# Optimization experiments

Measured on AMD Instinct MI355X. Metric: run time of the kernel, lower is better.

## Reference

```python
import jax, jax.numpy as jnp
import numpy as np

B, H, W, C = 8, 64, 64, 256
NH, WS, SS = 8, 8, 4
HD = C // NH          # head dim 32
N = WS * WS           # 64 tokens per window
NW = (H // WS) * (W // WS)  # 64 windows
MLP = 4 * C


def _rel_index():
    ch = np.arange(WS)
    coords = np.stack(np.meshgrid(ch, ch, indexing='ij')).reshape(2, -1)  # [2, N]
    rel = (coords[:, :, None] - coords[:, None, :]).transpose(1, 2, 0)   # [N, N, 2]
    rel[:, :, 0] += WS - 1
    rel[:, :, 1] += WS - 1
    rel[:, :, 0] *= 2 * WS - 1
    return jnp.asarray(rel.sum(-1))  # [N, N] indices into table

REL_IDX = _rel_index()


def _attn_mask():
    # standard Swin shifted-window mask: [nW, N, N] with 0 / -100
    img = np.zeros((H, W))
    slices = (slice(0, -WS), slice(-WS, -SS), slice(-SS, None))
    cnt = 0
    for hs in slices:
        for ws_ in slices:
            img[hs, ws_] = cnt
            cnt += 1
    m = img.reshape(H // WS, WS, W // WS, WS).transpose(0, 2, 1, 3).reshape(-1, N)
    diff = m[:, None, :] - m[:, :, None]
    return jnp.asarray(np.where(diff != 0, -100.0, 0.0).astype(np.float32))

MASK = _attn_mask()


def setup_inputs() -> dict:
    key = jax.random.key(0)
    ks = jax.random.split(key, 8)
    s = 0.02
    return {
        'hidden_states': jax.random.normal(ks[0], (B, H * W, C), jnp.float32),
        'ln1_g': jnp.ones((C,), jnp.float32),
        'ln1_b': jnp.zeros((C,), jnp.float32),
        'wq': jax.random.normal(ks[1], (C, C), jnp.float32) * s,
        'bq': jnp.zeros((C,), jnp.float32),
        'wk': jax.random.normal(ks[2], (C, C), jnp.float32) * s,
        'bk': jnp.zeros((C,), jnp.float32),
        'wv': jax.random.normal(ks[3], (C, C), jnp.float32) * s,
        'bv': jnp.zeros((C,), jnp.float32),
        'rel_table': jax.random.normal(ks[4], ((2 * WS - 1) ** 2, NH), jnp.float32) * s,
        'wo': jax.random.normal(ks[5], (C, C), jnp.float32) * s,
        'bo': jnp.zeros((C,), jnp.float32),
        'ln2_g': jnp.ones((C,), jnp.float32),
        'ln2_b': jnp.zeros((C,), jnp.float32),
        'w1': jax.random.normal(ks[6], (MLP, C), jnp.float32) * s,
        'b1': jnp.zeros((MLP,), jnp.float32),
        'w2': jax.random.normal(ks[7], (C, MLP), jnp.float32) * s,
        'b2': jnp.zeros((C,), jnp.float32),
    }


def _ln(x, g, b):
    mu = x.mean(-1, keepdims=True)
    var = x.var(-1, keepdims=True)
    return (x - mu) * jax.lax.rsqrt(var + 1e-5) * g + b


def reference(hidden_states, ln1_g, ln1_b, wq, bq, wk, bk, wv, bv, rel_table,
              wo, bo, ln2_g, ln2_b, w1, b1, w2, b2):
    shortcut = hidden_states
    x = _ln(hidden_states, ln1_g, ln1_b).reshape(B, H, W, C)
    # cyclic shift
    x = jnp.roll(x, (-SS, -SS), axis=(1, 2))
    # window partition -> [B*nW, N, C]
    xw = x.reshape(B, H // WS, WS, W // WS, WS, C).transpose(0, 1, 3, 2, 4, 5).reshape(-1, N, C)
    q = (xw @ wq.T + bq).reshape(-1, N, NH, HD).transpose(0, 2, 1, 3)
    k = (xw @ wk.T + bk).reshape(-1, N, NH, HD).transpose(0, 2, 1, 3)
    v = (xw @ wv.T + bv).reshape(-1, N, NH, HD).transpose(0, 2, 1, 3)
    scores = jnp.einsum('bhnd,bhmd->bhnm', q, k) / np.float32(np.sqrt(HD))
    bias = rel_table[REL_IDX]                 # [N, N, NH] gathered bias
    scores = scores + bias.transpose(2, 0, 1)[None]
    scores = scores.reshape(B, NW, NH, N, N) + MASK[None, :, None]
    probs = jax.nn.softmax(scores, axis=-1).reshape(-1, NH, N, N)
    ctx = jnp.einsum('bhnm,bhmd->bnhd', probs, v).reshape(-1, N, C)
    attn_out = ctx @ wo.T + bo                # SelfOutput dense
    # window reverse + reverse shift
    x = attn_out.reshape(B, H // WS, W // WS, WS, WS, C).transpose(0, 1, 3, 2, 4, 5).reshape(B, H, W, C)
    x = jnp.roll(x, (SS, SS), axis=(1, 2)).reshape(B, H * W, C)
    hidden = shortcut + x
    y = _ln(hidden, ln2_g, ln2_b)
    y = jax.nn.gelu(y @ w1.T + b1, approximate=False) @ w2.T + b2
    return hidden + y
```

## Files before the change

### kernel.cpp

```cpp
#include <hip/hip_runtime.h>
#include <hip/hip_bf16.h>
#include <math.h>

__device__ __forceinline__ unsigned short f2bf(float f) {
    union { float f; unsigned u; } c; c.f = f;
    unsigned r = c.u + 0x7fffu + ((c.u >> 16) & 1u);
    return (unsigned short)(r >> 16);
}
__device__ __forceinline__ float bfu(unsigned short u) {
    union { unsigned x; float f; } c; c.x = ((unsigned)u) << 16; return c.f;
}
__device__ __forceinline__ float gelu_t(float x) {
    float z = x * (1.59576912f + 0.07135481f * x * x);
    return x / (1.0f + __expf(-z));
}

typedef __bf16 bf16x8_t __attribute__((ext_vector_type(8)));
typedef float  f32x4_t  __attribute__((ext_vector_type(4)));
typedef unsigned short u16x8 __attribute__((ext_vector_type(8)));

#define AS1 __attribute__((address_space(1)))
#define AS3 __attribute__((address_space(3)))
__device__ __forceinline__ void g2lds16(const void* g, void* l) {
    __builtin_amdgcn_global_load_lds((const AS1 unsigned int*)g, (AS3 unsigned int*)l, 16, 0, 0);
}

__global__ void cvt_all(const float* __restrict__ wq, const float* __restrict__ wk,
                        const float* __restrict__ wv, const float* __restrict__ wo,
                        const float* __restrict__ w1, const float* __restrict__ w2,
                        const float* __restrict__ bq, const float* __restrict__ bk,
                        const float* __restrict__ bv, float* __restrict__ bqkv,
                        unsigned short* __restrict__ qkvp, unsigned short* __restrict__ wop,
                        unsigned short* __restrict__ w1p, unsigned short* __restrict__ w2p) {
    int fid = blockIdx.x * 256 + threadIdx.x;
    if (fid >= 98304) {
        int i = fid - 98304;
        if (i < 768) bqkv[i] = (i < 256) ? bq[i] : (i < 512 ? bk[i - 256] : bv[i - 512]);
        return;
    }
    const float* src; unsigned short* dst; int n, kf, KC;
    if (fid < 24576) {
        n = fid >> 5; kf = fid & 31; KC = 8;
        const float* w = (n < 256) ? wq : (n < 512 ? wk : wv);
        src = w + (size_t)(n & 255) * 256 + kf * 8; dst = qkvp;
    } else if (fid < 32768) {
        int fi = fid - 24576; n = fi >> 5; kf = fi & 31; KC = 8;
        src = wo + (size_t)n * 256 + kf * 8; dst = wop;
    } else if (fid < 65536) {
        int fi = fid - 32768; n = fi >> 5; kf = fi & 31; KC = 8;
        src = w1 + (size_t)n * 256 + kf * 8; dst = w1p;
    } else {
        int fi = fid - 65536; n = fi >> 7; kf = fi & 127; KC = 32;
        src = w2 + (size_t)n * 1024 + kf * 8; dst = w2p;
    }
    size_t oidx = (size_t)(((n >> 7) * KC + (kf >> 2)) * 4096)
                + ((n >> 4) & 7) * 512 + (kf & 3) * 128 + (n & 15) * 8;
    float4 a = *(const float4*)(src);
    float4 b = *(const float4*)(src + 4);
    u16x8 o = { f2bf(a.x), f2bf(a.y), f2bf(a.z), f2bf(a.w),
                f2bf(b.x), f2bf(b.y), f2bf(b.z), f2bf(b.w) };
    *(u16x8*)(dst + oidx) = o;
}

template<int GATHER, int BF16IN>
__global__ void ln_kernel(const void* __restrict__ xv, const float* __restrict__ g,
                          const float* __restrict__ b, unsigned short* __restrict__ out) {
    int row  = blockIdx.x * 4 + (threadIdx.x >> 6);
    int lane = threadIdx.x & 63;
    int src;
    if (GATHER) {
        int bb = row >> 12;
        int rem = row & 4095;
        int winid = rem >> 6, tok = rem & 63;
        int wi = winid >> 3, wj = winid & 7;
        int ii = tok >> 3,  jj = tok & 7;
        int hh = (wi * 8 + ii + 4) & 63;
        int ww = (wj * 8 + jj + 4) & 63;
        src = (bb << 12) + hh * 64 + ww;
    } else {
        src = row;
    }
    float4 v;
    if (BF16IN) {
        ushort4 u = *(const ushort4*)((const unsigned short*)xv + (size_t)src * 256 + lane * 4);
        v.x = bfu(u.x); v.y = bfu(u.y); v.z = bfu(u.z); v.w = bfu(u.w);
    } else {
        v = *(const float4*)((const float*)xv + (size_t)src * 256 + lane * 4);
    }
    float s  = v.x + v.y + v.z + v.w;
    float s2 = v.x*v.x + v.y*v.y + v.z*v.z + v.w*v.w;
    #pragma unroll
    for (int off = 32; off > 0; off >>= 1) {
        s  += __shfl_xor(s,  off, 64);
        s2 += __shfl_xor(s2, off, 64);
    }
    float mean = s * (1.0f / 256.0f);
    float var  = s2 * (1.0f / 256.0f) - mean * mean;
    float rstd = rsqrtf(var + 1e-5f);
    int c0 = lane * 4;
    float4 gg  = *(const float4*)(g + c0);
    float4 bb4 = *(const float4*)(b + c0);
    ushort4 o;
    o.x = f2bf((v.x - mean) * rstd * gg.x + bb4.x);
    o.y = f2bf((v.y - mean) * rstd * gg.y + bb4.y);
    o.z = f2bf((v.z - mean) * rstd * gg.z + bb4.z);
    o.w = f2bf((v.w - mean) * rstd * gg.w + bb4.w);
    *(ushort4*)(out + (size_t)row * 256 + c0) = o;
}

template<int MODE, int K>
__global__ __launch_bounds__(256, 4) void gemm_tile(
        const unsigned short* __restrict__ A,
        const unsigned short* __restrict__ Bp,
        const float* __restrict__ bias,
        int M, int N,
        unsigned short* __restrict__ obf,
        float* __restrict__ of32,
        const void* __restrict__ addp) {
    __shared__ __align__(16) char smem_raw[64 * 132 * 4];
    unsigned short* sm = (unsigned short*)smem_raw;
    float* cst = (float*)smem_raw;
    const int t = threadIdx.x;
    const int lane = t & 63, wave = t >> 6;
    const int m0 = blockIdx.x * 128, n0 = blockIdx.y * 128;
    const int wm = (wave >> 1) * 64, wn = (wave & 1) * 64;
    const int lr = lane & 15, kg = lane >> 4;

    f32x4_t acc[4][4];
    #pragma unroll
    for (int i = 0; i < 4; ++i)
        #pragma unroll
        for (int j = 0; j < 4; ++j) { acc[i][j][0]=0.f; acc[i][j][1]=0.f; acc[i][j][2]=0.f; acc[i][j][3]=0.f; }

    const unsigned short* ga  = A  + (size_t)(m0 + (t >> 2)) * K + (t & 3) * 8;
    const unsigned short* gbp = Bp + (size_t)blockIdx.y * (K / 32) * 4096 + t * 8;
    unsigned short* lA = sm + t * 8;
    unsigned short* lB = sm + 4096 + t * 8;

    const int NT = K / 32;
    g2lds16(ga,                  lA);
    g2lds16(ga + (size_t)64 * K, lA + 2048);
    g2lds16(gbp,                 lB);
    g2lds16(gbp + 2048,          lB + 2048);
    __syncthreads();

    #pragma unroll
    for (int k = 0; k < NT; ++k) {
        const int cur = k & 1;
        if (k + 1 < NT) {
            const int nx = cur ^ 1;
            g2lds16(ga + (k + 1) * 32,                  lA + nx * 8192);
            g2lds16(ga + (size_t)64 * K + (k + 1) * 32, lA + nx * 8192 + 2048);
            g2lds16(gbp + (size_t)(k + 1) * 4096,        lB + nx * 8192);
            g2lds16(gbp + (size_t)(k + 1) * 4096 + 2048, lB + nx * 8192 + 2048);
        }
        const unsigned short* Ab = sm + cur * 8192;
        const unsigned short* Bb = Ab + 4096;
        bf16x8_t af[4], bfr[4];
        #pragma unroll
        for (int i = 0; i < 4; ++i)
            af[i] = *(const bf16x8_t*)&Ab[(wm + i * 16 + lr) * 32 + kg * 8];
        #pragma unroll
        for (int j = 0; j < 4; ++j)
            bfr[j] = *(const bf16x8_t*)&Bb[(((wave & 1) * 4 + j) * 64 + lane) * 8];
        #pragma unroll
        for (int i = 0; i < 4; ++i)
            #pragma unroll
            for (int j = 0; j < 4; ++j)
                acc[i][j] = __builtin_amdgcn_mfma_f32_16x16x32_bf16(af[i], bfr[j], acc[i][j], 0, 0, 0);
        __syncthreads();
    }

    #pragma unroll
    for (int pass = 0; pass < 2; ++pass) {
        if (pass) __syncthreads();
        if ((wave >> 1) == pass) {
            float* cw = cst + (kg * 4) * 132 + wn + lr;
            #pragma unroll
            for (int i = 0; i < 4; ++i)
                #pragma unroll
                for (int j = 0; j < 4; ++j)
                    #pragma unroll
                    for (int e = 0; e < 4; ++e)
                        cw[(i * 16 + e) * 132 + j * 16] = acc[i][j][e];
        }
        __syncthreads();
        const int rr = t >> 4;
        const int ch = t & 15;
        if (MODE == 0 || MODE == 1) {
            #pragma unroll
            for (int c = 0; c < 4; ++c) {
                int r = rr + c * 16;
                int grow = m0 + pass * 64 + r;
                const float* cr = cst + r * 132 + ch * 8;
                const float* bp = bias + n0 + ch * 8;
                float4 a   = *(const float4*)(cr);
                float4 b4  = *(const float4*)(cr + 4);
                float4 ba  = *(const float4*)(bp);
                float4 bb4 = *(const float4*)(bp + 4);
                float x0 = a.x + ba.x,  x1 = a.y + ba.y,  x2 = a.z + ba.z,  x3 = a.w + ba.w;
                float x4 = b4.x + bb4.x, x5 = b4.y + bb4.y, x6 = b4.z + bb4.z, x7 = b4.w + bb4.w;
                if (MODE == 1) {
                    x0 = gelu_t(x0); x1 = gelu_t(x1); x2 = gelu_t(x2); x3 = gelu_t(x3);
                    x4 = gelu_t(x4); x5 = gelu_t(x5); x6 = gelu_t(x6); x7 = gelu_t(x7);
                }
                u16x8 o = { f2bf(x0), f2bf(x1), f2bf(x2), f2bf(x3),
                            f2bf(x4), f2bf(x5), f2bf(x6), f2bf(x7) };
                *(u16x8*)(obf + (size_t)grow * N + n0 + ch * 8) = o;
            }
        } else if (MODE == 2) {
            #pragma unroll
            for (int c = 0; c < 4; ++c) {
                int r = rr + c * 16;
                int grow = m0 + pass * 64 + r;
                int bb_ = grow >> 12, rem = grow & 4095;
                int winid = rem >> 6, tok = rem & 63;
                int wi = winid >> 3, wj = winid & 7;
                int ii = tok >> 3,  jj = tok & 7;
                int hh = (wi * 8 + ii + 4) & 63;
                int ww = (wj * 8 + jj + 4) & 63;
                size_t drow = (size_t)(bb_ << 12) + hh * 64 + ww;
                const float* cr = cst + r * 132 + ch * 8;
                const float* bp = bias + n0 + ch * 8;
                const float* res = (const float*)addp + drow * N + n0 + ch * 8;
                float4 a   = *(const float4*)(cr);
                float4 b4  = *(const float4*)(cr + 4);
                float4 ba  = *(const float4*)(bp);
                float4 bb4 = *(const float4*)(bp + 4);
                float4 ra  = *(const float4*)(res);
                float4 rb  = *(const float4*)(res + 4);
                u16x8 o = { f2bf(a.x + ba.x + ra.x),  f2bf(a.y + ba.y + ra.y),
                            f2bf(a.z + ba.z + ra.z),  f2bf(a.w + ba.w + ra.w),
                            f2bf(b4.x + bb4.x + rb.x), f2bf(b4.y + bb4.y + rb.y),
                            f2bf(b4.z + bb4.z + rb.z), f2bf(b4.w + bb4.w + rb.w) };
                *(u16x8*)(obf + drow * N + n0 + ch * 8) = o;
            }
        } else {
            #pragma unroll
            for (int c = 0; c < 8; ++c) {
                int r = rr + (c & 3) * 16;
                int grow = m0 + pass * 64 + r;
                int chunk = ch + (c >> 2) * 16;
                const float* cr = cst + r * 132 + chunk * 4;
                const float* bp = bias + n0 + chunk * 4;
                const unsigned short* res = (const unsigned short*)addp + (size_t)grow * N + n0 + chunk * 4;
                float4 a  = *(const float4*)(cr);
                float4 ba = *(const float4*)(bp);
                ushort4 rv = *(const ushort4*)(res);
                float4 o1 = { bfu(rv.x) + a.x + ba.x,  bfu(rv.y) + a.y + ba.y,
                              bfu(rv.z) + a.z + ba.z,  bfu(rv.w) + a.w + ba.w };
                *(float4*)(of32 + (size_t)grow * N + n0 + chunk * 4) = o1;
            }
        }
    }
}

#define PR 72
#define VR 72
__global__ void __launch_bounds__(256) attn_mfma(
        const unsigned short* __restrict__ qkv,
        const float* __restrict__ relt,
        unsigned short* __restrict__ ctx) {
    __shared__ float rs[1800];
    __shared__ unsigned short Pl[4][64 * PR];
    __shared__ unsigned short Vt[4][32 * VR];

    int t = threadIdx.x;
    int lane = t & 63, wave = t >> 6;
    for (int i = t; i < 1800; i += 256) rs[i] = relt[i];
    __syncthreads();

    int wh = blockIdx.x * 4 + wave;
    int wg = wh >> 3, h = wh & 7;
    int win = wg & 63;
    int ln = lane & 15, quad = lane >> 4;

    unsigned short* P = &Pl[wave][0];
    unsigned short* V = &Vt[wave][0];
    const unsigned short* base = qkv + (size_t)wg * 64 * 768 + h * 32;

    union BF8 { bf16x8_t v; unsigned short s[8]; };
    {
        const bf16x8_t* vp = (const bf16x8_t*)(base + (size_t)lane * 768 + 512);
        BF8 vv[4];
        #pragma unroll
        for (int c = 0; c < 4; ++c) vv[c].v = vp[c];
        #pragma unroll
        for (int c = 0; c < 4; ++c)
            #pragma unroll
            for (int e = 0; e < 8; ++e)
                V[(c * 8 + e) * VR + lane] = vv[c].s[e];
    }

    bf16x8_t qa[4], kb[4];
    #pragma unroll
    for (int i = 0; i < 4; ++i)
        qa[i] = *(const bf16x8_t*)(base + (size_t)(i * 16 + ln) * 768 + quad * 8);
    #pragma unroll
    for (int j = 0; j < 4; ++j)
        kb[j] = *(const bf16x8_t*)(base + (size_t)(j * 16 + ln) * 768 + 256 + quad * 8);

    f32x4_t acc[4][4];
    #pragma unroll
    for (int i = 0; i < 4; ++i)
        #pragma unroll
        for (int j = 0; j < 4; ++j) { acc[i][j][0]=0.f; acc[i][j][1]=0.f; acc[i][j][2]=0.f; acc[i][j][3]=0.f; }
    #pragma unroll
    for (int i = 0; i < 4; ++i)
        #pragma unroll
        for (int j = 0; j < 4; ++j)
            acc[i][j] = __builtin_amdgcn_mfma_f32_16x16x32_bf16(qa[i], kb[j], acc[i][j], 0, 0, 0);

    const float scale = 0.17677669529663687f;
    int wi = win >> 3, wj = win & 7;
    int mjv = ln & 7;
    int regm[4], mi[4];
    #pragma unroll
    for (int j = 0; j < 4; ++j) {
        mi[j] = j * 2 + (ln >> 3);
        int hm = wi * 8 + mi[j], wm = wj * 8 + mjv;
        regm[j] = (hm < 56 ? 0 : (hm < 60 ? 1 : 2)) * 3 + (wm < 56 ? 0 : (wm < 60 ? 1 : 2));
    }
    float inv[4][4];
    #pragma unroll
    for (int i = 0; i < 4; ++i) {
        #pragma unroll
        for (int e = 0; e < 4; ++e) {
            int q = i * 16 + quad * 4 + e;
            int ti = q >> 3, tj = q & 7;
            int hn = wi * 8 + ti, wn = wj * 8 + tj;
            int regn = (hn < 56 ? 0 : (hn < 60 ? 1 : 2)) * 3 + (wn < 56 ? 0 : (wn < 60 ? 1 : 2));
            float sum = 0.f;
            #pragma unroll
            for (int j = 0; j < 4; ++j) {
                float bv = rs[((ti - mi[j] + 7) * 15 + (tj - mjv + 7)) * 8 + h];
                float sv = acc[i][j][e] * scale + bv + (regm[j] != regn ? -100.f : 0.f);
                float p = __expf(sv);
                sum += p;
                P[q * PR + j * 16 + ln] = f2bf(p);
            }
            #pragma unroll
            for (int off = 1; off < 16; off <<= 1) sum += __shfl_xor(sum, off, 64);
            inv[i][e] = 1.0f / sum;
        }
    }
    __syncthreads();

    bf16x8_t vb[2][2];
    #pragma unroll
    for (int jd = 0; jd < 2; ++jd)
        #pragma unroll
        for (int kc = 0; kc < 2; ++kc)
            vb[jd][kc] = *(const bf16x8_t*)&V[(jd * 16 + ln) * VR + kc * 32 + quad * 8];
    f32x4_t occ[4][2];
    #pragma unroll
    for (int i = 0; i < 4; ++i)
        #pragma unroll
        for (int jd = 0; jd < 2; ++jd) { occ[i][jd][0]=0.f; occ[i][jd][1]=0.f; occ[i][jd][2]=0.f; occ[i][jd][3]=0.f; }
    #pragma unroll
    for (int i = 0; i < 4; ++i) {
        #pragma unroll
        for (int kc = 0; kc < 2; ++kc) {
            bf16x8_t pf = *(const bf16x8_t*)&P[(i * 16 + ln) * PR + kc * 32 + quad * 8];
            occ[i][0] = __builtin_amdgcn_mfma_f32_16x16x32_bf16(pf, vb[0][kc], occ[i][0], 0, 0, 0);
            occ[i][1] = __builtin_amdgcn_mfma_f32_16x16x32_bf16(pf, vb[1][kc], occ[i][1], 0, 0, 0);
        }
    }

    unsigned short* cbase = ctx + (size_t)wg * 64 * 256 + h * 32;
    #pragma unroll
    for (int i = 0; i < 4; ++i)
        #pragma unroll
        for (int e = 0; e < 4; ++e) {
            int q = i * 16 + quad * 4 + e;
            #pragma unroll
            for (int jd = 0; jd < 2; ++jd)
                cbase[(size_t)q * 256 + jd * 16 + ln] = f2bf(occ[i][jd][e] * inv[i][e]);
        }
}

extern "C" void kernel_launch(void* const* d_in, const int* in_sizes, int n_in,
                              void* d_out, int out_size, void* d_ws, size_t ws_size,
                              hipStream_t stream) {
    const float* hs   = (const float*)d_in[0];
    const float* ln1g = (const float*)d_in[1];
    const float* ln1b = (const float*)d_in[2];
    const float* wq   = (const float*)d_in[3];
    const float* bq   = (const float*)d_in[4];
    const float* wk   = (const float*)d_in[5];
    const float* bk   = (const float*)d_in[6];
    const float* wv   = (const float*)d_in[7];
    const float* bv   = (const float*)d_in[8];
    const float* relt = (const float*)d_in[9];
    const float* wo   = (const float*)d_in[10];
    const float* bo   = (const float*)d_in[11];
    const float* ln2g = (const float*)d_in[12];
    const float* ln2b = (const float*)d_in[13];
    const float* w1   = (const float*)d_in[14];
    const float* b1   = (const float*)d_in[15];
    const float* w2   = (const float*)d_in[16];
    const float* b2   = (const float*)d_in[17];
    float* out = (float*)d_out;

    const size_t NTOK = 32768;
    size_t off = 0;
    auto carve = [&](size_t bytes) { void* p = (char*)d_ws + off; off += (bytes + 255) & ~(size_t)255; return p; };
    unsigned short* wqkv_p = (unsigned short*)carve(768ull * 256 * 2);
    unsigned short* wo_p   = (unsigned short*)carve(65536ull * 2);
    unsigned short* w1p    = (unsigned short*)carve(262144ull * 2);
    unsigned short* w2p    = (unsigned short*)carve(262144ull * 2);
    float*          bqkv   = (float*)carve(768ull * 4);
    unsigned short* hiddenb= (unsigned short*)carve(NTOK * 256 * 2);
    unsigned short* xw     = (unsigned short*)carve(NTOK * 256 * 2);
    unsigned short* qkvb   = (unsigned short*)carve(NTOK * 768 * 2);
    unsigned short* cx     = (unsigned short*)carve(NTOK * 256 * 2);
    unsigned short* h1 = qkvb;
    unsigned short* yb = xw;

    cvt_all<<<385, 256, 0, stream>>>(wq, wk, wv, wo, w1, w2, bq, bk, bv, bqkv,
                                     wqkv_p, wo_p, w1p, w2p);

    ln_kernel<1, 0><<<8192, 256, 0, stream>>>(hs, ln1g, ln1b, xw);

    gemm_tile<0, 256><<<dim3(256, 6), 256, 0, stream>>>(xw, wqkv_p, bqkv, 32768, 768, qkvb, nullptr, nullptr);

    attn_mfma<<<1024, 256, 0, stream>>>(qkvb, relt, cx);

    gemm_tile<2, 256><<<dim3(256, 2), 256, 0, stream>>>(cx, wo_p, bo, 32768, 256, hiddenb, nullptr, hs);

    ln_kernel<0, 1><<<8192, 256, 0, stream>>>(hiddenb, ln2g, ln2b, yb);

    gemm_tile<1, 256><<<dim3(256, 8), 256, 0, stream>>>(yb, w1p, b1, 32768, 1024, h1, nullptr, nullptr);

    gemm_tile<3, 1024><<<dim3(256, 2), 256, 0, stream>>>(h1, w2p, b2, 32768, 256, nullptr, out, hiddenb);
}
```

Baseline: 246.1 us.

## Fold LN2 into the MLP up-projection GEMM and write head-major QKV layout

After: 259.9 us. 5.6% more time.

```diff
diff --git a/kernel.cpp b/kernel.cpp
--- a/kernel.cpp
+++ b/kernel.cpp
@@ -28,6 +28,7 @@
 __global__ void cvt_all(const float* __restrict__ wq, const float* __restrict__ wk,
                         const float* __restrict__ wv, const float* __restrict__ wo,
                         const float* __restrict__ w1, const float* __restrict__ w2,
+                        const float* __restrict__ ln2g,
                         const float* __restrict__ bq, const float* __restrict__ bk,
                         const float* __restrict__ bv, float* __restrict__ bqkv,
                         unsigned short* __restrict__ qkvp, unsigned short* __restrict__ wop,
@@ -38,7 +39,7 @@
         if (i < 768) bqkv[i] = (i < 256) ? bq[i] : (i < 512 ? bk[i - 256] : bv[i - 512]);
         return;
     }
-    const float* src; unsigned short* dst; int n, kf, KC;
+    const float* src; unsigned short* dst; int n, kf, KC, isw1 = 0;
     if (fid < 24576) {
         n = fid >> 5; kf = fid & 31; KC = 8;
         const float* w = (n < 256) ? wq : (n < 512 ? wk : wv);
@@ -48,7 +49,7 @@
         src = wo + (size_t)n * 256 + kf * 8; dst = wop;
     } else if (fid < 65536) {
         int fi = fid - 32768; n = fi >> 5; kf = fi & 31; KC = 8;
-        src = w1 + (size_t)n * 256 + kf * 8; dst = w1p;
+        src = w1 + (size_t)n * 256 + kf * 8; dst = w1p; isw1 = 1;
     } else {
         int fi = fid - 65536; n = fi >> 7; kf = fi & 127; KC = 32;
         src = w2 + (size_t)n * 1024 + kf * 8; dst = w2p;
@@ -57,9 +58,34 @@
                 + ((n >> 4) & 7) * 512 + (kf & 3) * 128 + (n & 15) * 8;
     float4 a = *(const float4*)(src);
     float4 b = *(const float4*)(src + 4);
+    if (isw1) {
+        int k0 = kf * 8;
+        float4 g0 = *(const float4*)(ln2g + k0);
+        float4 g1 = *(const float4*)(ln2g + k0 + 4);
+        a.x *= g0.x; a.y *= g0.y; a.z *= g0.z; a.w *= g0.w;
+        b.x *= g1.x; b.y *= g1.y; b.z *= g1.z; b.w *= g1.w;
+    }
     u16x8 o = { f2bf(a.x), f2bf(a.y), f2bf(a.z), f2bf(a.w),
                 f2bf(b.x), f2bf(b.y), f2bf(b.z), f2bf(b.w) };
     *(u16x8*)(dst + oidx) = o;
+}
+
+__global__ void prep_mlp(const float* __restrict__ w1, const float* __restrict__ ln2g,
+                         const float* __restrict__ ln2b, const float* __restrict__ b1,
+                         float* __restrict__ s1, float* __restrict__ b1p) {
+    int n = blockIdx.x * 256 + threadIdx.x;
+    const float* wr = w1 + (size_t)n * 256;
+    float ss = 0.f, sb = 0.f;
+    #pragma unroll 4
+    for (int k = 0; k < 256; k += 4) {
+        float4 w = *(const float4*)(wr + k);
+        float4 g = *(const float4*)(ln2g + k);
+        float4 b = *(const float4*)(ln2b + k);
+        ss += w.x * g.x + w.y * g.y + w.z * g.z + w.w * g.w;
+        sb += w.x * b.x + w.y * b.y + w.z * b.z + w.w * b.w;
+    }
+    s1[n] = ss;
+    b1p[n] = b1[n] + sb;
 }
 
 template<int GATHER, int BF16IN>
@@ -117,14 +143,35 @@
         unsigned short* __restrict__ obf,
         float* __restrict__ of32,
         const void* __restrict__ addp) {
-    __shared__ __align__(16) char smem_raw[64 * 132 * 4];
+    __shared__ __align__(16) char smem_raw[34816];
     unsigned short* sm = (unsigned short*)smem_raw;
     float* cst = (float*)smem_raw;
+    float* stats = (float*)(smem_raw + 33792);
     const int t = threadIdx.x;
     const int lane = t & 63, wave = t >> 6;
     const int m0 = blockIdx.x * 128, n0 = blockIdx.y * 128;
     const int wm = (wave >> 1) * 64, wn = (wave & 1) * 64;
     const int lr = lane & 15, kg = lane >> 4;
+
+    if (MODE == 5) {
+        const unsigned short* xp = A + (size_t)(m0 + (t >> 1)) * 256 + (t & 1) * 128;
+        float s = 0.f, s2 = 0.f;
+        #pragma unroll
+        for (int f = 0; f < 16; ++f) {
+            u16x8 xf = *(const u16x8*)(xp + f * 8);
+            #pragma unroll
+            for (int e = 0; e < 8; ++e) { float v = bfu(xf[e]); s += v; s2 += v * v; }
+        }
+        s  += __shfl_xor(s, 1, 64);
+        s2 += __shfl_xor(s2, 1, 64);
+        if ((t & 1) == 0) {
+            float mean = s * (1.0f / 256.0f);
+            float var  = s2 * (1.0f / 256.0f) - mean * mean;
+            float rst  = rsqrtf(var + 1e-5f);
+            stats[t >> 1] = rst;
+            stats[128 + (t >> 1)] = mean * rst;
+        }
+    }
 
     f32x4_t acc[4][4];
     #pragma unroll
@@ -187,7 +234,7 @@
         __syncthreads();
         const int rr = t >> 4;
         const int ch = t & 15;
-        if (MODE == 0 || MODE == 1) {
+        if (MODE == 0) {
             #pragma unroll
             for (int c = 0; c < 4; ++c) {
                 int r = rr + c * 16;
@@ -198,12 +245,53 @@
                 float4 b4  = *(const float4*)(cr + 4);
                 float4 ba  = *(const float4*)(bp);
                 float4 bb4 = *(const float4*)(bp + 4);
-                float x0 = a.x + ba.x,  x1 = a.y + ba.y,  x2 = a.z + ba.z,  x3 = a.w + ba.w;
-                float x4 = b4.x + bb4.x, x5 = b4.y + bb4.y, x6 = b4.z + bb4.z, x7 = b4.w + bb4.w;
-                if (MODE == 1) {
-                    x0 = gelu_t(x0); x1 = gelu_t(x1); x2 = gelu_t(x2); x3 = gelu_t(x3);
-                    x4 = gelu_t(x4); x5 = gelu_t(x5); x6 = gelu_t(x6); x7 = gelu_t(x7);
-                }
+                u16x8 o = { f2bf(a.x + ba.x),  f2bf(a.y + ba.y),  f2bf(a.z + ba.z),  f2bf(a.w + ba.w),
+                            f2bf(b4.x + bb4.x), f2bf(b4.y + bb4.y), f2bf(b4.z + bb4.z), f2bf(b4.w + bb4.w) };
+                *(u16x8*)(obf + (size_t)grow * N + n0 + ch * 8) = o;
+            }
+        } else if (MODE == 4) {
+            #pragma unroll
+            for (int c = 0; c < 4; ++c) {
+                int r = rr + c * 16;
+                int grow = m0 + pass * 64 + r;
+                int wgq = grow >> 6, tok = grow & 63;
+                int cc = n0 + ch * 8;
+                int sel = cc >> 8, hh = (cc >> 5) & 7, d = cc & 31;
+                size_t dst = ((size_t)(wgq * 3 + sel) * 8 + hh) * 2048 + tok * 32 + d;
+                const float* cr = cst + r * 132 + ch * 8;
+                const float* bp = bias + cc;
+                float4 a   = *(const float4*)(cr);
+                float4 b4  = *(const float4*)(cr + 4);
+                float4 ba  = *(const float4*)(bp);
+                float4 bb4 = *(const float4*)(bp + 4);
+                u16x8 o = { f2bf(a.x + ba.x),  f2bf(a.y + ba.y),  f2bf(a.z + ba.z),  f2bf(a.w + ba.w),
+                            f2bf(b4.x + bb4.x), f2bf(b4.y + bb4.y), f2bf(b4.z + bb4.z), f2bf(b4.w + bb4.w) };
+                *(u16x8*)(obf + dst) = o;
+            }
+        } else if (MODE == 5) {
+            #pragma unroll
+            for (int c = 0; c < 4; ++c) {
+                int r = rr + c * 16;
+                int grow = m0 + pass * 64 + r;
+                float rst = stats[pass * 64 + r];
+                float mrs = stats[128 + pass * 64 + r];
+                const float* cr = cst + r * 132 + ch * 8;
+                const float* bp = bias + n0 + ch * 8;
+                const float* sp = (const float*)addp + n0 + ch * 8;
+                float4 a   = *(const float4*)(cr);
+                float4 b4  = *(const float4*)(cr + 4);
+                float4 ba  = *(const float4*)(bp);
+                float4 bb4 = *(const float4*)(bp + 4);
+                float4 sa  = *(const float4*)(sp);
+                float4 sb  = *(const float4*)(sp + 4);
+                float x0 = gelu_t(rst * a.x - mrs * sa.x + ba.x);
+                float x1 = gelu_t(rst * a.y - mrs * sa.y + ba.y);
+                float x2 = gelu_t(rst * a.z - mrs * sa.z + ba.z);
+                float x3 = gelu_t(rst * a.w - mrs * sa.w + ba.w);
+                float x4 = gelu_t(rst * b4.x - mrs * sb.x + bb4.x);
+                float x5 = gelu_t(rst * b4.y - mrs * sb.y + bb4.y);
+                float x6 = gelu_t(rst * b4.z - mrs * sb.z + bb4.z);
+                float x7 = gelu_t(rst * b4.w - mrs * sb.w + bb4.w);
                 u16x8 o = { f2bf(x0), f2bf(x1), f2bf(x2), f2bf(x3),
                             f2bf(x4), f2bf(x5), f2bf(x6), f2bf(x7) };
                 *(u16x8*)(obf + (size_t)grow * N + n0 + ch * 8) = o;
@@ -277,11 +365,13 @@
 
     unsigned short* P = &Pl[wave][0];
     unsigned short* V = &Vt[wave][0];
-    const unsigned short* base = qkv + (size_t)wg * 64 * 768 + h * 32;
+    const unsigned short* bq_ = qkv + ((size_t)(wg * 3 + 0) * 8 + h) * 2048;
+    const unsigned short* bk_ = qkv + ((size_t)(wg * 3 + 1) * 8 + h) * 2048;
+    const unsigned short* bv_ = qkv + ((size_t)(wg * 3 + 2) * 8 + h) * 2048;
 
     union BF8 { bf16x8_t v; unsigned short s[8]; };
     {
-        const bf16x8_t* vp = (const bf16x8_t*)(base + (size_t)lane * 768 + 512);
+        const bf16x8_t* vp = (const bf16x8_t*)(bv_ + (size_t)lane * 32);
         BF8 vv[4];
         #pragma unroll
         for (int c = 0; c < 4; ++c) vv[c].v = vp[c];
@@ -295,10 +385,10 @@
     bf16x8_t qa[4], kb[4];
     #pragma unroll
     for (int i = 0; i < 4; ++i)
-        qa[i] = *(const bf16x8_t*)(base + (size_t)(i * 16 + ln) * 768 + quad * 8);
+        qa[i] = *(const bf16x8_t*)(bq_ + (size_t)(i * 16 + ln) * 32 + quad * 8);
     #pragma unroll
     for (int j = 0; j < 4; ++j)
-        kb[j] = *(const bf16x8_t*)(base + (size_t)(j * 16 + ln) * 768 + 256 + quad * 8);
+        kb[j] = *(const bf16x8_t*)(bk_ + (size_t)(j * 16 + ln) * 32 + quad * 8);
 
     f32x4_t acc[4][4];
     #pragma unroll
@@ -410,27 +500,27 @@
     unsigned short* w1p    = (unsigned short*)carve(262144ull * 2);
     unsigned short* w2p    = (unsigned short*)carve(262144ull * 2);
     float*          bqkv   = (float*)carve(768ull * 4);
+    float*          s1w    = (float*)carve(1024ull * 4);
+    float*          b1w    = (float*)carve(1024ull * 4);
     unsigned short* hiddenb= (unsigned short*)carve(NTOK * 256 * 2);
     unsigned short* xw     = (unsigned short*)carve(NTOK * 256 * 2);
     unsigned short* qkvb   = (unsigned short*)carve(NTOK * 768 * 2);
     unsigned short* cx     = (unsigned short*)carve(NTOK * 256 * 2);
     unsigned short* h1 = qkvb;
-    unsigned short* yb = xw;
-
-    cvt_all<<<385, 256, 0, stream>>>(wq, wk, wv, wo, w1, w2, bq, bk, bv, bqkv,
+
+    cvt_all<<<385, 256, 0, stream>>>(wq, wk, wv, wo, w1, w2, ln2g, bq, bk, bv, bqkv,
                                      wqkv_p, wo_p, w1p, w2p);
+    prep_mlp<<<4, 256, 0, stream>>>(w1, ln2g, ln2b, b1, s1w, b1w);
 
     ln_kernel<1, 0><<<8192, 256, 0, stream>>>(hs, ln1g, ln1b, xw);
 
-    gemm_tile<0, 256><<<dim3(256, 6), 256, 0, stream>>>(xw, wqkv_p, bqkv, 32768, 768, qkvb, nullptr, nullptr);
+    gemm_tile<4, 256><<<dim3(256, 6), 256, 0, stream>>>(xw, wqkv_p, bqkv, 32768, 768, qkvb, nullptr, nullptr);
 
     attn_mfma<<<1024, 256, 0, stream>>>(qkvb, relt, cx);
 
     gemm_tile<2, 256><<<dim3(256, 2), 256, 0, stream>>>(cx, wo_p, bo, 32768, 256, hiddenb, nullptr, hs);
 
-    ln_kernel<0, 1><<<8192, 256, 0, stream>>>(hiddenb, ln2g, ln2b, yb);
-
-    gemm_tile<1, 256><<<dim3(256, 8), 256, 0, stream>>>(yb, w1p, b1, 32768, 1024, h1, nullptr, nullptr);
+    gemm_tile<5, 256><<<dim3(256, 8), 256, 0, stream>>>(hiddenb, w1p, b1w, 32768, 1024, h1, nullptr, s1w);
 
     gemm_tile<3, 1024><<<dim3(256, 2), 256, 0, stream>>>(h1, w2p, b2, 32768, 256, nullptr, out, hiddenb);
 }
```
